# Optimization experiments

Measured on AMD Instinct MI355X. Metric: run time of the kernel, lower is better.

The kernel has to match this reference:

```python
import jax, jax.numpy as jnp
import numpy as np

B, H, W, C = 4, 256, 256, 64
KH = KW = 3
UNITS = 1          # forced: conv in-channels must equal kernel in-channels (see notes)
G = 1              # num_deformable_group
HP, WP = H + 2, W + 2  # 'same' padding for 3x3 stride-1: pad 1 each side


def _conv_indices(h, w):
    """Replicates tf.image.extract_image_patches('SAME') on an index grid:
    border patches read zero-padded coordinates. Returns int [h, w, 9]."""
    yg, xg = jnp.meshgrid(jnp.arange(h), jnp.arange(w), indexing='ij')
    yp = jnp.pad(yg, 1)
    xp = jnp.pad(xg, 1)
    ys = jnp.stack([yp[ky:ky + h, kx:kx + w] for ky in range(KH) for kx in range(KW)], -1)
    xs = jnp.stack([xp[ky:ky + h, kx:kx + w] for ky in range(KH) for kx in range(KW)], -1)
    return ys, xs


def setup_inputs() -> dict:
    key = jax.random.key(0)
    k1, k2, k3, k4 = jax.random.split(key, 4)
    input_fp = jax.random.normal(k1, (B, H, W, C), jnp.float32)
    gt_mask = jax.random.randint(k2, (1, H, W, 1), 0, 2).astype(jnp.float32)
    offset = jax.random.normal(k3, (B, H, W, UNITS * KH * KW * 2), jnp.float32)
    fan_in = KH * KW * C
    kernel = jax.random.normal(k4, (KH, KW, C, UNITS), jnp.float32) / np.float32(np.sqrt(fan_in))
    bias = jnp.zeros((UNITS,), jnp.float32)
    return {"input_fp": input_fp, "gt_mask": gt_mask, "offset": offset,
            "kernel": kernel, "bias": bias}


def reference(input_fp, gt_mask, offset, kernel, bias):
    pad = ((0, 0), (1, 1), (1, 1), (0, 0))
    fp = jnp.pad(input_fp, pad)                 # [B, HP, WP, C]
    mk = jnp.pad(gt_mask, pad)[0, :, :, 0]      # [HP, WP]; original tiles this over batch/channels

    off = offset.reshape(B, H, W, UNITS * KH * KW, 2)
    y_off, x_off = off[..., 0], off[..., 1]     # [B, H, W, 9]

    yi, xi = _conv_indices(H, W)                # [H, W, 9] int
    yf = yi[None].astype(jnp.float32)           # [1, H, W, 9], broadcasts over batch
    xf = xi[None].astype(jnp.float32)

    # mask at base sample points and at offset sample points
    p_mask = mk[yi, xi][None]                                        # [1, H, W, 9]
    yo = jnp.clip(jnp.floor(yf + y_off).astype(jnp.int32), 0, HP - 1)
    xo = jnp.clip(jnp.floor(xf + x_off).astype(jnp.int32), 0, WP - 1)
    p_mask_off = mk[yo, xo]                                          # [B, H, W, 9]
    diff = (p_mask != p_mask_off).astype(jnp.float32)

    y = jnp.clip(yf + y_off * diff, 0.0, H - 1.0)
    x = jnp.clip(xf + x_off * diff, 0.0, W - 1.0)
    y0 = jnp.floor(y).astype(jnp.int32)
    x0 = jnp.floor(x).astype(jnp.int32)

    b = jnp.arange(B)[:, None, None, None]
    pixels = fp[b, y0, x0]                      # [B, H, W, 9, C] nearest-floor sampling
    # [B,H,W,kh,kw,G,C] -> [B,H,kh,W,kw,G,C] -> [B, H*kh, W*kw, G*C]
    pixels = pixels.reshape(B, H, W, KH, KW, G, C)
    pixels = pixels.transpose(0, 1, 3, 2, 4, 5, 6)
    pixels = pixels.reshape(B, H * KH, W * KW, G * C)   # feat_in_group = units//G = 1, tile is a no-op

    out = jax.lax.conv_general_dilated(
        pixels, kernel, window_strides=(KH, KW), padding='SAME',
        dimension_numbers=('NHWC', 'HWIO', 'NHWC'))      # [B, H, W, UNITS]
    return out + bias
```

## Files before the change

### kernel.cpp

```cpp
#include <hip/hip_runtime.h>

#define HW 256
#define CH 64
#define NPIX (4 * HW * HW)
#define ENC_BYTES ((size_t)NPIX * 24)
#define DM_OFF ((size_t)8 << 20)
#define DM_BYTES ((size_t)NPIX * 36)
#define WS_NEED (DM_OFF + DM_BYTES)

__global__ __launch_bounds__(256, 4) void DeformA2_kernel(
    const float* __restrict__ gt,
    const float* __restrict__ off,
    unsigned short* __restrict__ enc)
{
    const int tid = threadIdx.x;
    const int bid = blockIdx.x;
    const int vb = (bid & 7) * 128 + (bid >> 3);
    const int p = vb * 256 + tid;
    const int i = (p >> 8) & 255;
    const int j = p & 255;

    const float* op = off + (size_t)p * 18;
    const float4 q0 = *(const float4*)(op + 0);
    const float4 q1 = *(const float4*)(op + 4);
    const float4 q2 = *(const float4*)(op + 8);
    const float4 q3 = *(const float4*)(op + 12);
    const float2 q4 = *(const float2*)(op + 16);
    float oy[9], ox[9];
    oy[0]=q0.x; ox[0]=q0.y; oy[1]=q0.z; ox[1]=q0.w;
    oy[2]=q1.x; ox[2]=q1.y; oy[3]=q1.z; ox[3]=q1.w;
    oy[4]=q2.x; ox[4]=q2.y; oy[5]=q2.z; ox[5]=q2.w;
    oy[6]=q3.x; ox[6]=q3.y; oy[7]=q3.z; ox[7]=q3.w;
    oy[8]=q4.x; ox[8]=q4.y;

    unsigned w[5];
    #pragma unroll
    for (int k = 0; k < 5; ++k) w[k] = 0u;

    #pragma unroll
    for (int tap = 0; tap < 9; ++tap) {
        const int ky = tap / 3, kx = tap - ky * 3;
        const int iy = i + ky - 1, ix = j + kx - 1;
        const bool interior = (iy >= 0) & (iy < HW) & (ix >= 0) & (ix < HW);
        const int yi = interior ? iy : 0;
        const int xi = interior ? ix : 0;
        const float p_mask = (yi >= 1 && xi >= 1) ? gt[(yi - 1) * HW + (xi - 1)] : 0.f;

        const float yf = (float)yi, xf = (float)xi;
        const float yof = fminf(fmaxf(floorf(yf + oy[tap]), 0.f), 257.f);
        const float xof = fminf(fmaxf(floorf(xf + ox[tap]), 0.f), 257.f);
        const int yo = (int)yof, xo = (int)xof;
        const float p_mask_off = (yo >= 1 && yo <= HW && xo >= 1 && xo <= HW)
                                 ? gt[(yo - 1) * HW + (xo - 1)] : 0.f;
        const float diff = (p_mask != p_mask_off) ? 1.f : 0.f;
        const float y = fminf(fmaxf(yf + oy[tap] * diff, 0.f), 255.f);
        const float x = fminf(fmaxf(xf + ox[tap] * diff, 0.f), 255.f);
        const int y0 = (int)y, x0 = (int)x;
        const unsigned e = (unsigned)((y0 << 8) | x0);
        w[tap >> 1] |= e << ((tap & 1) * 16);
    }

    unsigned short* ep = enc + (size_t)p * 12u;
    *(uint2*)(ep + 0) = make_uint2(w[0], w[1]);
    *(uint2*)(ep + 4) = make_uint2(w[2], w[3]);
    *(uint2*)(ep + 8) = make_uint2(w[4], 0u);
}

template <int CTRL>
__device__ __forceinline__ float dpp_ror_add(float x) {
    int xi = __builtin_bit_cast(int, x);
    int yi = __builtin_amdgcn_update_dpp(0, xi, CTRL, 0xF, 0xF, false);
    return x + __builtin_bit_cast(float, yi);
}
#define ROR1 0x121
#define ROR2 0x122
#define ROR4 0x124
#define ROR8 0x128

__global__ __launch_bounds__(256, 4) void DeformD5_kernel(
    const float* __restrict__ inp,
    const float* __restrict__ ker,
    float* __restrict__ dm)
{
    const int lane = threadIdx.x & 63;
    const int wave = threadIdx.x >> 6;
    const int t = lane & 15;
    const int g = lane >> 4;

    float4 wk[9];
    #pragma unroll
    for (int k = 0; k < 9; ++k)
        wk[k] = *(const float4*)(ker + k * 64 + t * 4);

    const int pxbase = blockIdx.x * 128 + wave * 32;

    #pragma unroll
    for (int it = 0; it < 4; ++it) {
        const int pA = pxbase + it * 8 + g;
        const int pB = pA + 4;
        const float4 v0 = *(const float4*)(inp + (size_t)pA * 64 + t * 4);
        const float4 v1 = *(const float4*)(inp + (size_t)pB * 64 + t * 4);

        float da[9], db[9];
        #pragma unroll
        for (int k = 0; k < 9; ++k) {
            const float4 w = wk[k];
            da[k] = v0.x * w.x + v0.y * w.y + v0.z * w.z + v0.w * w.w;
            db[k] = v1.x * w.x + v1.y * w.y + v1.z * w.z + v1.w * w.w;
        }
        #pragma unroll
        for (int k = 0; k < 9; ++k) {
            da[k] = dpp_ror_add<ROR8>(da[k]);
            da[k] = dpp_ror_add<ROR4>(da[k]);
            da[k] = dpp_ror_add<ROR2>(da[k]);
            da[k] = dpp_ror_add<ROR1>(da[k]);
            db[k] = dpp_ror_add<ROR8>(db[k]);
            db[k] = dpp_ror_add<ROR4>(db[k]);
            db[k] = dpp_ror_add<ROR2>(db[k]);
            db[k] = dpp_ror_add<ROR1>(db[k]);
        }
        float sa = 0.f, sb = 0.f;
        #pragma unroll
        for (int k = 8; k >= 0; --k) {
            sa = (t == k) ? da[k] : sa;
            sb = (t == k) ? db[k] : sb;
        }
        if (t < 9) {
            dm[(size_t)t * NPIX + pA] = sa;
            dm[(size_t)t * NPIX + pB] = sb;
        }
    }
}

__global__ __launch_bounds__(256, 8) void DeformC3_kernel(
    const unsigned short* __restrict__ enc,
    const float* __restrict__ dm,
    const float* __restrict__ bias,
    float* __restrict__ out)
{
    const int tid = threadIdx.x;
    const int bid = blockIdx.x;
    const int vb = (bid & 7) * 128 + (bid >> 3);
    const int p = vb * 256 + tid;
    const size_t bbase = (size_t)(p >> 16) << 16;

    const uint2* e = (const uint2*)(enc + (size_t)p * 12u);
    const uint2 eA = e[0];
    const uint2 eB = e[1];
    const unsigned eC = *(const unsigned*)(e + 2);

    unsigned en[9];
    en[0] = eA.x & 0xffffu; en[1] = eA.x >> 16;
    en[2] = eA.y & 0xffffu; en[3] = eA.y >> 16;
    en[4] = eB.x & 0xffffu; en[5] = eB.x >> 16;
    en[6] = eB.y & 0xffffu; en[7] = eB.y >> 16;
    en[8] = eC & 0xffffu;

    float v[9];
    int msk = 0;
    #pragma unroll
    for (int k = 0; k < 9; ++k) {
        const int yy = (int)(en[k] >> 8);
        const int xx = (int)(en[k] & 255u);
        const bool valid = (yy >= 1) & (xx >= 1);
        msk |= (int)valid << k;
        const int idx = valid ? ((yy - 1) * HW + (xx - 1)) : 0;
        v[k] = dm[(size_t)k * NPIX + bbase + idx];
    }
    float sum = 0.f;
    #pragma unroll
    for (int k = 0; k < 9; ++k)
        sum += ((msk >> k) & 1) ? v[k] : 0.f;

    out[p] = sum + bias[0];
}

__global__ __launch_bounds__(256, 6) void DeformFallback_kernel(
    const float* __restrict__ inp, const float* __restrict__ gt,
    const float* __restrict__ off, const float* __restrict__ ker,
    const float* __restrict__ bias, float* __restrict__ out)
{
    __shared__ float wlds[576];
    const int tid = threadIdx.x;
    if (tid < 144) ((float4*)wlds)[tid] = ((const float4*)ker)[tid];

    const int lane = tid & 63;
    const int wave = tid >> 6;
    const int q16  = lane & 48;
    const int t    = lane & 15;

    const int bid = blockIdx.x;
    const int vb  = (bid & 7) * 2048 + (bid >> 3);

    const int p = vb * 16 + wave * 4 + (q16 >> 4);
    const int b = p >> 16;
    const int i = (p >> 8) & 255;
    const int j = p & 255;
    const float* inb = inp + (long)b * (HW * HW * CH);

    int pack = 0;
    if (t < 9) {
        const int tap = t;
        const int ky = tap / 3, kx = tap - ky * 3;
        int iy = i + ky - 1, ix = j + kx - 1;
        bool interior = (iy >= 0) & (iy < HW) & (ix >= 0) & (ix < HW);
        int yi = interior ? iy : 0;
        int xi = interior ? ix : 0;
        float p_mask = (yi >= 1 && xi >= 1) ? gt[(yi - 1) * HW + (xi - 1)] : 0.f;
        float2 o2 = *(const float2*)(off + (long)p * 18 + 2 * tap);
        float yf = (float)yi, xf = (float)xi;
        float yof = fminf(fmaxf(floorf(yf + o2.x), 0.f), 257.f);
        float xof = fminf(fmaxf(floorf(xf + o2.y), 0.f), 257.f);
        int yo = (int)yof, xo = (int)xof;
        float p_mask_off = (yo >= 1 && yo <= HW && xo >= 1 && xo <= HW)
                           ? gt[(yo - 1) * HW + (xo - 1)] : 0.f;
        float diff = (p_mask != p_mask_off) ? 1.f : 0.f;
        float y = fminf(fmaxf(yf + o2.x * diff, 0.f), 255.f);
        float x = fminf(fmaxf(xf + o2.y * diff, 0.f), 255.f);
        int y0 = (int)y;
        int x0 = (int)x;
        bool valid = (y0 >= 1) & (x0 >= 1);
        int eoff = ((y0 - 1) * HW + (x0 - 1)) * CH;
        pack = valid ? eoff : -1;
    }

    int pk[9];
    #pragma unroll
    for (int k = 0; k < 9; ++k) pk[k] = __shfl(pack, q16 + k);

    float4 v[9];
    #pragma unroll
    for (int k = 0; k < 9; ++k) {
        int eo2 = pk[k] >= 0 ? pk[k] : 0;
        v[k] = *(const float4*)(inb + eo2 + t * 4);
    }

    __syncthreads();

    float acc = 0.f;
    #pragma unroll
    for (int k = 0; k < 9; ++k) {
        float s = pk[k] >= 0 ? 1.f : 0.f;
        float4 w = ((const float4*)wlds)[k * 16 + t];
        float d = v[k].x * w.x + v[k].y * w.y + v[k].z * w.z + v[k].w * w.w;
        acc = fmaf(s, d, acc);
    }

    acc += __shfl_xor(acc, 8);
    acc += __shfl_xor(acc, 4);
    acc += __shfl_xor(acc, 2);
    acc += __shfl_xor(acc, 1);
    if (t == 0) out[p] = acc + bias[0];
}

extern "C" void kernel_launch(void* const* d_in, const int* in_sizes, int n_in,
                              void* d_out, int out_size, void* d_ws, size_t ws_size,
                              hipStream_t stream) {
    const float* inp  = (const float*)d_in[0];
    const float* gt   = (const float*)d_in[1];
    const float* off  = (const float*)d_in[2];
    const float* ker  = (const float*)d_in[3];
    const float* bias = (const float*)d_in[4];
    float* out = (float*)d_out;

    if (d_ws != nullptr && ws_size >= WS_NEED) {
        unsigned short* enc = (unsigned short*)d_ws;
        float* dm = (float*)((char*)d_ws + DM_OFF);
        DeformA2_kernel<<<1024, 256, 0, stream>>>(gt, off, enc);
        DeformD5_kernel<<<2048, 256, 0, stream>>>(inp, ker, dm);
        DeformC3_kernel<<<1024, 256, 0, stream>>>(enc, dm, bias, out);
    } else {
        DeformFallback_kernel<<<16384, 256, 0, stream>>>(inp, gt, off, ker, bias, out);
    }
}
```

Measured before the change: 124.2 us.

## Fuse index computation into gather kernel with LDS-resident packed mask bits

The separate offset/mask index kernel, which wrote 24-byte encoded indices per pixel, is removed and its logic is folded into the final gather kernel. A small new kernel packs the gt mask into a 64K-bit bitmap with ballot, and each gather block copies it into shared memory so the mask lookups become LDS bit tests instead of global float reads. This removes the intermediate encoded-index round trip through global memory. In exchange, every block reloads 8 KB of bitmap and hits a barrier, and the gather kernel gets heavier per thread.

Measured after the change: 122.0 us. About the same (-1.7%).

```diff
diff --git a/kernel.cpp b/kernel.cpp
--- a/kernel.cpp
+++ b/kernel.cpp
@@ -3,22 +3,112 @@
 #define HW 256
 #define CH 64
 #define NPIX (4 * HW * HW)
-#define ENC_BYTES ((size_t)NPIX * 24)
 #define DM_OFF ((size_t)8 << 20)
 #define DM_BYTES ((size_t)NPIX * 36)
 #define WS_NEED (DM_OFF + DM_BYTES)
 
-__global__ __launch_bounds__(256, 4) void DeformA2_kernel(
+__global__ __launch_bounds__(256) void DeformP_kernel(
     const float* __restrict__ gt,
+    unsigned* __restrict__ bits)
+{
+    const int g = blockIdx.x * 256 + threadIdx.x;
+    const unsigned long long m = __ballot(gt[g] != 0.0f);
+    if ((threadIdx.x & 63) == 0) {
+        const int w = g >> 5;
+        bits[w]     = (unsigned)(m & 0xffffffffu);
+        bits[w + 1] = (unsigned)(m >> 32);
+    }
+}
+
+template <int CTRL>
+__device__ __forceinline__ float dpp_ror_add(float x) {
+    int xi = __builtin_bit_cast(int, x);
+    int yi = __builtin_amdgcn_update_dpp(0, xi, CTRL, 0xF, 0xF, false);
+    return x + __builtin_bit_cast(float, yi);
+}
+#define ROR1 0x121
+#define ROR2 0x122
+#define ROR4 0x124
+#define ROR8 0x128
+
+__global__ __launch_bounds__(256, 4) void DeformD5_kernel(
+    const float* __restrict__ inp,
+    const float* __restrict__ ker,
+    float* __restrict__ dm)
+{
+    const int lane = threadIdx.x & 63;
+    const int wave = threadIdx.x >> 6;
+    const int t = lane & 15;
+    const int g = lane >> 4;
+
+    float4 wk[9];
+    #pragma unroll
+    for (int k = 0; k < 9; ++k)
+        wk[k] = *(const float4*)(ker + k * 64 + t * 4);
+
+    const int pxbase = blockIdx.x * 128 + wave * 32;
+
+    #pragma unroll
+    for (int it = 0; it < 4; ++it) {
+        const int pA = pxbase + it * 8 + g;
+        const int pB = pA + 4;
+        const float4 v0 = *(const float4*)(inp + (size_t)pA * 64 + t * 4);
+        const float4 v1 = *(const float4*)(inp + (size_t)pB * 64 + t * 4);
+
+        float da[9], db[9];
+        #pragma unroll
+        for (int k = 0; k < 9; ++k) {
+            const float4 w = wk[k];
+            da[k] = v0.x * w.x + v0.y * w.y + v0.z * w.z + v0.w * w.w;
+            db[k] = v1.x * w.x + v1.y * w.y + v1.z * w.z + v1.w * w.w;
+        }
+        #pragma unroll
+        for (int k = 0; k < 9; ++k) {
+            da[k] = dpp_ror_add<ROR8>(da[k]);
+            da[k] = dpp_ror_add<ROR4>(da[k]);
+            da[k] = dpp_ror_add<ROR2>(da[k]);
+            da[k] = dpp_ror_add<ROR1>(da[k]);
+            db[k] = dpp_ror_add<ROR8>(db[k]);
+            db[k] = dpp_ror_add<ROR4>(db[k]);
+            db[k] = dpp_ror_add<ROR2>(db[k]);
+            db[k] = dpp_ror_add<ROR1>(db[k]);
+        }
+        float sa = 0.f, sb = 0.f;
+        #pragma unroll
+        for (int k = 8; k >= 0; --k) {
+            sa = (t == k) ? da[k] : sa;
+            sb = (t == k) ? db[k] : sb;
+        }
+        if (t < 9) {
+            dm[(size_t)t * NPIX + pA] = sa;
+            dm[(size_t)t * NPIX + pB] = sb;
+        }
+    }
+}
+
+__global__ __launch_bounds__(256, 4) void DeformACE_kernel(
     const float* __restrict__ off,
-    unsigned short* __restrict__ enc)
-{
+    const unsigned* __restrict__ bits,
+    const float* __restrict__ dm,
+    const float* __restrict__ bias,
+    float* __restrict__ out)
+{
+    __shared__ unsigned mlds[2048];
     const int tid = threadIdx.x;
+    {
+        const uint4* src = (const uint4*)bits;
+        uint4* dst = (uint4*)mlds;
+        dst[tid] = src[tid];
+        dst[tid + 256] = src[tid + 256];
+    }
+    __syncthreads();
+
     const int bid = blockIdx.x;
     const int vb = (bid & 7) * 128 + (bid >> 3);
     const int p = vb * 256 + tid;
     const int i = (p >> 8) & 255;
     const int j = p & 255;
+    const size_t bbase = (size_t)(p >> 16) << 16;
 
     const float* op = off + (size_t)p * 18;
     const float4 q0 = *(const float4*)(op + 0);
@@ -33,10 +123,7 @@
     oy[6]=q3.x; ox[6]=q3.y; oy[7]=q3.z; ox[7]=q3.w;
     oy[8]=q4.x; ox[8]=q4.y;
 
-    unsigned w[5];
-    #pragma unroll
-    for (int k = 0; k < 5; ++k) w[k] = 0u;
-
+    float sum = 0.f;
     #pragma unroll
     for (int tap = 0; tap < 9; ++tap) {
         const int ky = tap / 3, kx = tap - ky * 3;
@@ -44,134 +131,32 @@
         const bool interior = (iy >= 0) & (iy < HW) & (ix >= 0) & (ix < HW);
         const int yi = interior ? iy : 0;
         const int xi = interior ? ix : 0;
-        const float p_mask = (yi >= 1 && xi >= 1) ? gt[(yi - 1) * HW + (xi - 1)] : 0.f;
+
+        int pm = 0;
+        if (yi >= 1 && xi >= 1) {
+            const int bi = (yi - 1) * HW + (xi - 1);
+            pm = (int)((mlds[bi >> 5] >> (bi & 31)) & 1u);
+        }
 
         const float yf = (float)yi, xf = (float)xi;
         const float yof = fminf(fmaxf(floorf(yf + oy[tap]), 0.f), 257.f);
         const float xof = fminf(fmaxf(floorf(xf + ox[tap]), 0.f), 257.f);
         const int yo = (int)yof, xo = (int)xof;
-        const float p_mask_off = (yo >= 1 && yo <= HW && xo >= 1 && xo <= HW)
-                                 ? gt[(yo - 1) * HW + (xo - 1)] : 0.f;
-        const float diff = (p_mask != p_mask_off) ? 1.f : 0.f;
+        int pmo = 0;
+        if (yo >= 1 && yo <= HW && xo >= 1 && xo <= HW) {
+            const int bo = (yo - 1) * HW + (xo - 1);
+            pmo = (int)((mlds[bo >> 5] >> (bo & 31)) & 1u);
+        }
+        const float diff = (pm != pmo) ? 1.f : 0.f;
+
         const float y = fminf(fmaxf(yf + oy[tap] * diff, 0.f), 255.f);
         const float x = fminf(fmaxf(xf + ox[tap] * diff, 0.f), 255.f);
         const int y0 = (int)y, x0 = (int)x;
-        const unsigned e = (unsigned)((y0 << 8) | x0);
-        w[tap >> 1] |= e << ((tap & 1) * 16);
-    }
-
-    unsigned short* ep = enc + (size_t)p * 12u;
-    *(uint2*)(ep + 0) = make_uint2(w[0], w[1]);
-    *(uint2*)(ep + 4) = make_uint2(w[2], w[3]);
-    *(uint2*)(ep + 8) = make_uint2(w[4], 0u);
-}
-
-template <int CTRL>
-__device__ __forceinline__ float dpp_ror_add(float x) {
-    int xi = __builtin_bit_cast(int, x);
-    int yi = __builtin_amdgcn_update_dpp(0, xi, CTRL, 0xF, 0xF, false);
-    return x + __builtin_bit_cast(float, yi);
-}
-#define ROR1 0x121
-#define ROR2 0x122
-#define ROR4 0x124
-#define ROR8 0x128
-
-__global__ __launch_bounds__(256, 4) void DeformD5_kernel(
-    const float* __restrict__ inp,
-    const float* __restrict__ ker,
-    float* __restrict__ dm)
-{
-    const int lane = threadIdx.x & 63;
-    const int wave = threadIdx.x >> 6;
-    const int t = lane & 15;
-    const int g = lane >> 4;
-
-    float4 wk[9];
-    #pragma unroll
-    for (int k = 0; k < 9; ++k)
-        wk[k] = *(const float4*)(ker + k * 64 + t * 4);
-
-    const int pxbase = blockIdx.x * 128 + wave * 32;
-
-    #pragma unroll
-    for (int it = 0; it < 4; ++it) {
-        const int pA = pxbase + it * 8 + g;
-        const int pB = pA + 4;
-        const float4 v0 = *(const float4*)(inp + (size_t)pA * 64 + t * 4);
-        const float4 v1 = *(const float4*)(inp + (size_t)pB * 64 + t * 4);
-
-        float da[9], db[9];
-        #pragma unroll
-        for (int k = 0; k < 9; ++k) {
-            const float4 w = wk[k];
-            da[k] = v0.x * w.x + v0.y * w.y + v0.z * w.z + v0.w * w.w;
-            db[k] = v1.x * w.x + v1.y * w.y + v1.z * w.z + v1.w * w.w;
-        }
-        #pragma unroll
-        for (int k = 0; k < 9; ++k) {
-            da[k] = dpp_ror_add<ROR8>(da[k]);
-            da[k] = dpp_ror_add<ROR4>(da[k]);
-            da[k] = dpp_ror_add<ROR2>(da[k]);
-            da[k] = dpp_ror_add<ROR1>(da[k]);
-            db[k] = dpp_ror_add<ROR8>(db[k]);
-            db[k] = dpp_ror_add<ROR4>(db[k]);
-            db[k] = dpp_ror_add<ROR2>(db[k]);
-            db[k] = dpp_ror_add<ROR1>(db[k]);
-        }
-        float sa = 0.f, sb = 0.f;
-        #pragma unroll
-        for (int k = 8; k >= 0; --k) {
-            sa = (t == k) ? da[k] : sa;
-            sb = (t == k) ? db[k] : sb;
-        }
-        if (t < 9) {
-            dm[(size_t)t * NPIX + pA] = sa;
-            dm[(size_t)t * NPIX + pB] = sb;
-        }
-    }
-}
-
-__global__ __launch_bounds__(256, 8) void DeformC3_kernel(
-    const unsigned short* __restrict__ enc,
-    const float* __restrict__ dm,
-    const float* __restrict__ bias,
-    float* __restrict__ out)
-{
-    const int tid = threadIdx.x;
-    const int bid = blockIdx.x;
-    const int vb = (bid & 7) * 128 + (bid >> 3);
-    const int p = vb * 256 + tid;
-    const size_t bbase = (size_t)(p >> 16) << 16;
-
-    const uint2* e = (const uint2*)(enc + (size_t)p * 12u);
-    const uint2 eA = e[0];
-    const uint2 eB = e[1];
-    const unsigned eC = *(const unsigned*)(e + 2);
-
-    unsigned en[9];
-    en[0] = eA.x & 0xffffu; en[1] = eA.x >> 16;
-    en[2] = eA.y & 0xffffu; en[3] = eA.y >> 16;
-    en[4] = eB.x & 0xffffu; en[5] = eB.x >> 16;
-    en[6] = eB.y & 0xffffu; en[7] = eB.y >> 16;
-    en[8] = eC & 0xffffu;
-
-    float v[9];
-    int msk = 0;
-    #pragma unroll
-    for (int k = 0; k < 9; ++k) {
-        const int yy = (int)(en[k] >> 8);
-        const int xx = (int)(en[k] & 255u);
-        const bool valid = (yy >= 1) & (xx >= 1);
-        msk |= (int)valid << k;
-        const int idx = valid ? ((yy - 1) * HW + (xx - 1)) : 0;
-        v[k] = dm[(size_t)k * NPIX + bbase + idx];
-    }
-    float sum = 0.f;
-    #pragma unroll
-    for (int k = 0; k < 9; ++k)
-        sum += ((msk >> k) & 1) ? v[k] : 0.f;
-
+        const bool valid = (y0 >= 1) & (x0 >= 1);
+        const int idx = valid ? ((y0 - 1) * HW + (x0 - 1)) : 0;
+        const float v = dm[(size_t)tap * NPIX + bbase + idx];
+        sum += valid ? v : 0.f;
+    }
     out[p] = sum + bias[0];
 }
 
@@ -264,11 +249,11 @@
     float* out = (float*)d_out;
 
     if (d_ws != nullptr && ws_size >= WS_NEED) {
-        unsigned short* enc = (unsigned short*)d_ws;
+        unsigned* bits = (unsigned*)d_ws;
         float* dm = (float*)((char*)d_ws + DM_OFF);
-        DeformA2_kernel<<<1024, 256, 0, stream>>>(gt, off, enc);
+        DeformP_kernel<<<256, 256, 0, stream>>>(gt, bits);
         DeformD5_kernel<<<2048, 256, 0, stream>>>(inp, ker, dm);
-        DeformC3_kernel<<<1024, 256, 0, stream>>>(enc, dm, bias, out);
+        DeformACE_kernel<<<1024, 256, 0, stream>>>(off, bits, dm, bias, out);
     } else {
         DeformFallback_kernel<<<16384, 256, 0, stream>>>(inp, gt, off, ker, bias, out);
     }
```
